# Optimization experiments

Measured on AMD Instinct MI355X. Metric: run time of the kernel, lower is better.

The kernel has to match this reference:

```python
import jax, jax.numpy as jnp
import numpy as np

TEMPERATURE_F = 0.5


def setup_inputs() -> dict:
    key = jax.random.key(0)
    k1, k2, k3, k4, k5 = jax.random.split(key, 5)
    B, D, K = 4096, 128, 8192
    return {
        "h_i": jax.random.normal(k1, (B, D), dtype=jnp.float32),
        "h_j": jax.random.normal(k2, (B, D), dtype=jnp.float32),
        "sub_graph": jax.random.uniform(k3, (B, K), dtype=jnp.float32),
        "sub_x": jax.random.normal(k4, (B, D), dtype=jnp.float32),
        "all_x": jax.random.normal(k5, (K, D), dtype=jnp.float32),
    }


def _forward_feature(h_i, h_j):
    # NT-Xent contrastive loss (CrossEntropyLoss with label 0, reduction='sum', /N).
    B = h_i.shape[0]
    N = 2 * B
    h = jnp.concatenate([h_i, h_j], axis=0)           # [N, D]
    sim = (h @ h.T) / TEMPERATURE_F                   # [N, N]
    idx = jnp.arange(N)
    pos = sim[idx, (idx + B) % N]                     # positives: diag(sim, +B) ++ diag(sim, -B)
    # logits row i = [pos_i] ++ {sim[i,j] : j != i, j != i±B}. Since pos_i == sim[i, i±B],
    # the logsumexp over that row equals logsumexp over sim[i,:] with only the diagonal removed.
    sim_nodiag = jnp.where(jnp.eye(N, dtype=bool), -jnp.inf, sim)
    lse = jax.nn.logsumexp(sim_nodiag, axis=1)        # [N]
    return jnp.sum(lse - pos) / N


def _graph_loss(sub_graph, sub_x, all_x):
    # trace(X^T diag(r) X) = sum_i r_i * ||X_i||^2 ; trace(A^T G B) = sum(G * (A B^T)) = sum((G B) * A)
    r = jnp.sum(sub_graph, axis=1)                    # [M]
    c = jnp.sum(sub_graph, axis=0)                    # [K]
    t1 = jnp.sum(r * jnp.sum(sub_x * sub_x, axis=1))
    t2 = jnp.sum(c * jnp.sum(all_x * all_x, axis=1))
    t3 = jnp.sum((sub_graph @ all_x) * sub_x)         # trace(sub_x^T G all_x)
    M, K = sub_graph.shape
    return (t1 + t2 - 2.0 * t3) / (M * K)


def reference(h_i, h_j, sub_graph, sub_x, all_x):
    contrastive = _forward_feature(h_i, h_j)
    graph = _graph_loss(sub_graph, sub_x, all_x)
    return contrastive + graph
```

## Files before the change

### kernel.cpp

```cpp
#include <hip/hip_runtime.h>
#include <hip/hip_bf16.h>

typedef __attribute__((ext_vector_type(4)))  float f32x4;
typedef __attribute__((ext_vector_type(16))) float f32x16;
typedef __attribute__((ext_vector_type(8)))  short s16x8;
typedef unsigned short u16;
typedef unsigned int u32;

#define ALPHA 1.6986436f
#define LN2F  0.69314718056f
#define COFF  128.0f

__device__ __forceinline__ u16 f2bf(float x) {
  union { float f; u32 u; } v; v.f = x;
  u32 r = v.u + 0x7fffu + ((v.u >> 16) & 1u);
  return (u16)(r >> 16);
}

#if __has_builtin(__builtin_amdgcn_exp2f)
__device__ __forceinline__ float fexp2(float x) { return __builtin_amdgcn_exp2f(x); }
#else
__device__ __forceinline__ float fexp2(float x) { return exp2f(x); }
#endif
#if __has_builtin(__builtin_amdgcn_logf)
__device__ __forceinline__ float flog2(float x) { return __builtin_amdgcn_logf(x); }
#else
__device__ __forceinline__ float flog2(float x) { return log2f(x); }
#endif

__device__ __forceinline__ s16x8 cvt8(float4 a, float4 b) {
  union { u32 w[4]; s16x8 v; } u;
  asm("v_cvt_pk_bf16_f32 %0, %1, %2" : "=v"(u.w[0]) : "v"(a.x), "v"(a.y));
  asm("v_cvt_pk_bf16_f32 %0, %1, %2" : "=v"(u.w[1]) : "v"(a.z), "v"(a.w));
  asm("v_cvt_pk_bf16_f32 %0, %1, %2" : "=v"(u.w[2]) : "v"(b.x), "v"(b.y));
  asm("v_cvt_pk_bf16_f32 %0, %1, %2" : "=v"(u.w[3]) : "v"(b.z), "v"(b.w));
  return u.v;
}

__device__ __forceinline__ f32x16 mfma32(s16x8 a, s16x8 b, f32x16 c) {
  return __builtin_amdgcn_mfma_f32_32x32x16_bf16(a, b, c, 0, 0, 0);
}
__device__ __forceinline__ f32x16 zero16() {
  f32x16 z;
#pragma unroll
  for (int i = 0; i < 16; ++i) z[i] = 0.f;
  return z;
}
__device__ __forceinline__ void gl16(const void* g, void* l) {
  __builtin_amdgcn_global_load_lds(
      (const __attribute__((address_space(1))) u32*)g,
      (__attribute__((address_space(3))) u32*)l, 16, 0, 0);
}

__global__ __launch_bounds__(256)
void prep_all(const float* __restrict__ h_i, const float* __restrict__ h_j,
              const float* __restrict__ all_x, const float* __restrict__ subx,
              u16* __restrict__ hbf, u16* __restrict__ axG,
              float* __restrict__ nall, float* __restrict__ nsub,
              float* __restrict__ pos4) {
  __shared__ float tile[64 * 132];
  int bid = blockIdx.x, tid = threadIdx.x;
  if (bid < 512) {
    int t = bid * 256 + tid;
    int row = t >> 4, kb = t & 15;
    const float* src = (row < 4096 ? h_i + (size_t)row * 128
                                   : h_j + (size_t)(row - 4096) * 128) + kb * 8;
    float4 f0 = *(const float4*)(src);
    float4 f1 = *(const float4*)(src + 4);
    float4 sa = {ALPHA * f0.x, ALPHA * f0.y, ALPHA * f0.z, ALPHA * f0.w};
    float4 sb = {ALPHA * f1.x, ALPHA * f1.y, ALPHA * f1.z, ALPHA * f1.w};
    s16x8 o = cvt8(sa, sb);
    char* dst = (char*)hbf + (size_t)row * 256 + ((kb * 16) ^ ((row & 7) << 4));
    *(s16x8*)dst = o;
    if (row < 4096) {
      const float* srcj = h_j + (size_t)row * 128 + kb * 8;
      float4 g0 = *(const float4*)(srcj);
      float4 g1 = *(const float4*)(srcj + 4);
      float dp = f0.x * g0.x + f0.y * g0.y + f0.z * g0.z + f0.w * g0.w
               + f1.x * g1.x + f1.y * g1.y + f1.z * g1.z + f1.w * g1.w;
      dp += __shfl_xor(dp, 1, 64);
      dp += __shfl_xor(dp, 2, 64);
      dp += __shfl_xor(dp, 4, 64);
      dp += __shfl_xor(dp, 8, 64);
      if ((tid & 15) == 0) pos4[row] = 2.0f * dp;
    }
  } else if (bid < 640) {
    int ab = bid - 512;
    int k0 = ab * 64;
#pragma unroll
    for (int j = 0; j < 8; ++j) {
      int idx = (j * 256 + tid) * 4;
      int kk = idx >> 7, d = idx & 127;
      *(float4*)&tile[kk * 132 + d] = *(const float4*)&all_x[(size_t)(k0 + kk) * 128 + d];
    }
    __syncthreads();
    {
      int kk = tid >> 2, q = tid & 3;
      float s = 0.f;
#pragma unroll
      for (int dd = 0; dd < 32; ++dd) { float v = tile[kk * 132 + q * 32 + dd]; s += v * v; }
      s += __shfl_xor(s, 1, 64);
      s += __shfl_xor(s, 2, 64);
      if (q == 0) nall[k0 + kk] = s;
    }
#pragma unroll
    for (int half = 0; half < 2; ++half) {
      int tgt = half * 256 + tid;
      int f = tgt >> 7, d = tgt & 127;
      int kc = ab * 4 + f;
      u16* dp = axG + (size_t)kc * 2048 + d * 16;
      s16x8 o0, o1;
#pragma unroll
      for (int kk = 0; kk < 8; ++kk) {
        o0[kk] = (short)f2bf(tile[(f * 16 + kk) * 132 + d]);
        o1[kk] = (short)f2bf(tile[(f * 16 + 8 + kk) * 132 + d]);
      }
      ((s16x8*)dp)[0] = o0; ((s16x8*)dp)[1] = o1;
    }
  } else {
    int i = (bid - 640) * 256 + tid;
    const float* p = subx + (size_t)i * 128;
    float s = 0.f;
#pragma unroll
    for (int c = 0; c < 32; ++c) {
      float4 v = ((const float4*)p)[c];
      s += v.x * v.x + v.y * v.y + v.z * v.z + v.w * v.w;
    }
    nsub[i] = s;
  }
}

__global__ __launch_bounds__(256, 3)
void contrast_k(const u16* __restrict__ hbf, float* __restrict__ spart) {
  __shared__ char clds[2][8192];
  int bid = blockIdx.x, tid = threadIdx.x;
  int lane = tid & 63, w = tid >> 6, il = lane & 31, hi = lane >> 5;
  int rt = bid >> 5, oct = bid & 31;
  int C0 = oct * 256;
  int rowbase = rt * 256 + w * 64;
  s16x8 bf0[8], bf1[8];
#pragma unroll
  for (int rs = 0; rs < 2; ++rs) {
    int r = rowbase + rs * 32 + il;
    const char* rp = (const char*)hbf + (size_t)r * 256;
    int sw = (r & 7) << 4;
#pragma unroll
    for (int ks = 0; ks < 8; ++ks) {
      s16x8 v = *(const s16x8*)(rp + ((ks * 32 + hi * 16) ^ sw));
      if (rs == 0) bf0[ks] = v; else bf1[ks] = v;
    }
  }
  float s0 = 0.f, s1 = 0.f;
  auto stage = [&](int buf, int t) {
    const char* src = (const char*)hbf + (size_t)(C0 + t * 32) * 256 + tid * 16;
    char* dst = &clds[buf][0] + tid * 16;
    gl16(src, dst);
    gl16(src + 4096, dst + 4096);
  };
  stage(0, 0);
  __syncthreads();
  int cur = 0;
  for (int t = 0; t < 8; ++t) {
    if (t < 7) stage(cur ^ 1, t + 1);
    const char* basep = &clds[cur][0];
    s16x8 af[8];
#pragma unroll
    for (int ks = 0; ks < 8; ++ks)
      af[ks] = *(const s16x8*)(basep + il * 256 + ((ks * 32 + hi * 16) ^ ((il & 7) << 4)));
    f32x16 A0 = zero16(), A1 = zero16();
#pragma unroll
    for (int ks = 0; ks < 8; ++ks) {
      A0 = mfma32(af[ks], bf0[ks], A0);
      A1 = mfma32(af[ks], bf1[ks], A1);
    }
    int cb = C0 + t * 32;
    bool d0 = (cb == rowbase), d1 = (cb == rowbase + 32);
#pragma unroll
    for (int r = 0; r < 16; ++r) {
      int jc = (r & 3) + 8 * (r >> 2) + 4 * hi;
      float t0 = fexp2(A0[r] - COFF);
      float t1 = fexp2(A1[r] - COFF);
      if (d0 && jc == il) t0 = 0.f;
      if (d1 && jc == il) t1 = 0.f;
      s0 += t0; s1 += t1;
    }
    __syncthreads();
    cur ^= 1;
  }
  s0 += __shfl_xor(s0, 32, 64);
  s1 += __shfl_xor(s1, 32, 64);
  if (hi == 0) {
    spart[oct * 8192 + rowbase + il]      = s0;
    spart[oct * 8192 + rowbase + 32 + il] = s1;
  }
}

__global__ __launch_bounds__(256, 4)
void graph_k(const float* __restrict__ G, const float* __restrict__ subx,
             const u16* __restrict__ axG, const float* __restrict__ nall,
             const float* __restrict__ nsub, float* __restrict__ gpart) {
  __shared__ u16 gtile[2][32][64];
  __shared__ float wsum[4];
  int bid = blockIdx.x, tid = threadIdx.x;
  int lane = tid & 63, w = tid >> 6, il = lane & 31, hi = lane >> 5;
  int mt = bid >> 3, kq = bid & 7;
  int i0 = mt * 32, i = i0 + il;
  int kbase = kq * 1024;
  int srow = tid >> 3, s8 = tid & 7;
  const float* gsrc = G + (size_t)(i0 + srow) * 8192 + kbase + s8 * 4;
  const float* nsrc = nall + kbase + s8 * 4;
  int sw_w = (srow & 7) << 4;
  int wo0 = ((s8 << 3))      ^ sw_w;
  int wo1 = (64 | (s8 << 3)) ^ sw_w;
  char* wb0 = (char*)&gtile[0][srow][0];
  char* wb1 = (char*)&gtile[1][srow][0];
  int swr = (il & 7) << 4;
  const char* aBase = (const char*)axG + (size_t)(kq * 64) * 4096
                    + (size_t)w * 1024 + il * 32 + hi * 16;

  f32x16 acc = zero16();
  float rsum = 0.f, nsum = 0.f;
  float4 gA0, gB0, nA0, nB0, gA1, gB1, nA1, nB1;

#define GISSUE(S, GA, GB, NA, NB)                                      \
  { const float* p_ = gsrc + (S) * 64;                                 \
    GA = *(const float4*)p_; GB = *(const float4*)(p_ + 32);           \
    const float* n_ = nsrc + (S) * 64;                                 \
    NA = *(const float4*)n_; NB = *(const float4*)(n_ + 32); }

#define GCOMMIT(GA, GB, NA, NB, DSTB)                                              \
  { u32 c0_, c1_, c2_, c3_;                                                        \
    asm("v_cvt_pk_bf16_f32 %0, %1, %2" : "=v"(c0_) : "v"(GA.x), "v"(GA.y));        \
    asm("v_cvt_pk_bf16_f32 %0, %1, %2" : "=v"(c1_) : "v"(GA.z), "v"(GA.w));        \
    asm("v_cvt_pk_bf16_f32 %0, %1, %2" : "=v"(c2_) : "v"(GB.x), "v"(GB.y));        \
    asm("v_cvt_pk_bf16_f32 %0, %1, %2" : "=v"(c3_) : "v"(GB.z), "v"(GB.w));        \
    *(uint2*)((DSTB) + wo0) = make_uint2(c0_, c1_);                                \
    *(uint2*)((DSTB) + wo1) = make_uint2(c2_, c3_);                                \
    rsum += GA.x + GA.y + GA.z + GA.w + GB.x + GB.y + GB.z + GB.w;                 \
    nsum += GA.x * NA.x + GA.y * NA.y + GA.z * NA.z + GA.w * NA.w                  \
          + GB.x * NB.x + GB.y * NB.y + GB.z * NB.z + GB.w * NB.w; }

#define GBAR()                                                \
  asm volatile("s_waitcnt lgkmcnt(0)" ::: "memory");          \
  __builtin_amdgcn_sched_barrier(0);                          \
  __builtin_amdgcn_s_barrier();                               \
  __builtin_amdgcn_sched_barrier(0);

#define GSTEP(S, GA_I, GB_I, NA_I, NB_I, GA_O, GB_O, NA_O, NB_O, CURB, OTHB)       \
  { const char* aB_ = aBase + (size_t)((S) * 4) * 4096;                            \
    s16x8 aF0 = *(const s16x8*)(aB_);                                              \
    s16x8 aF1 = *(const s16x8*)(aB_ + 4096);                                       \
    s16x8 aF2 = *(const s16x8*)(aB_ + 8192);                                       \
    s16x8 aF3 = *(const s16x8*)(aB_ + 12288);                                      \
    if ((S) < 14) GISSUE((S) + 2, GA_I, GB_I, NA_I, NB_I);                         \
    const char* rb_ = (const char*)&gtile[CURB][il][0];                            \
    s16x8 B0 = *(const s16x8*)(rb_ + ((0 * 32 + hi * 16) ^ swr));                  \
    s16x8 B1 = *(const s16x8*)(rb_ + ((1 * 32 + hi * 16) ^ swr));                  \
    s16x8 B2 = *(const s16x8*)(rb_ + ((2 * 32 + hi * 16) ^ swr));                  \
    s16x8 B3 = *(const s16x8*)(rb_ + ((3 * 32 + hi * 16) ^ swr));                  \
    acc = mfma32(aF0, B0, acc);                                                    \
    acc = mfma32(aF1, B1, acc);                                                    \
    acc = mfma32(aF2, B2, acc);                                                    \
    acc = mfma32(aF3, B3, acc);                                                    \
    if ((S) < 15) GCOMMIT(GA_O, GB_O, NA_O, NB_O, (OTHB));                         \
    GBAR(); }

  GISSUE(0, gA0, gB0, nA0, nB0);
  GISSUE(1, gA1, gB1, nA1, nB1);
  GCOMMIT(gA0, gB0, nA0, nB0, wb0);
  GBAR();

  for (int sp = 0; sp < 8; ++sp) {
    int s = sp * 2;
    GSTEP(s,     gA0, gB0, nA0, nB0, gA1, gB1, nA1, nB1, 0, wb1);
    GSTEP(s + 1, gA1, gB1, nA1, nB1, gA0, gB0, nA0, nB0, 1, wb0);
  }
#undef GSTEP
#undef GBAR
#undef GCOMMIT
#undef GISSUE

  float p = rsum * nsub[i0 + srow] + nsum;
  const float* sxr = subx + (size_t)i * 128 + w * 32 + hi * 4;
#pragma unroll
  for (int rq = 0; rq < 4; ++rq) {
    float4 sx = *(const float4*)(sxr + rq * 8);
    p -= 2.0f * (acc[rq * 4 + 0] * sx.x + acc[rq * 4 + 1] * sx.y +
                 acc[rq * 4 + 2] * sx.z + acc[rq * 4 + 3] * sx.w);
  }
#pragma unroll
  for (int d = 1; d < 64; d <<= 1) p += __shfl_xor(p, d, 64);
  if (lane == 0) wsum[w] = p;
  __syncthreads();
  if (tid == 0) gpart[bid] = wsum[0] + wsum[1] + wsum[2] + wsum[3];
}

__global__ __launch_bounds__(256)
void epilogue1(const float* __restrict__ spart, const float* __restrict__ pos4,
               float* __restrict__ cpart) {
  int tid = threadIdx.x;
  int row = blockIdx.x * 256 + tid;
  float S = 0.f;
#pragma unroll
  for (int o = 0; o < 32; ++o) S += spart[o * 8192 + row];
  float c = LN2F * (COFF + flog2(S)) - pos4[row & 4095];
#pragma unroll
  for (int d = 1; d < 64; d <<= 1) c += __shfl_xor(c, d, 64);
  __shared__ float ws4[4];
  int l = tid & 63, w = tid >> 6;
  if (l == 0) ws4[w] = c;
  __syncthreads();
  if (tid == 0) cpart[blockIdx.x] = ws4[0] + ws4[1] + ws4[2] + ws4[3];
}

__global__ __launch_bounds__(256)
void final_sum(const float* __restrict__ cpart, const float* __restrict__ gpart,
               float* __restrict__ out) {
  int tid = threadIdx.x;
  double gd = 0.0;
  for (int idx = tid; idx < 1024; idx += 256) gd += (double)gpart[idx];
  double cd = (tid < 32) ? (double)cpart[tid] : 0.0;
#pragma unroll
  for (int d = 1; d < 64; d <<= 1) {
    cd += __shfl_xor(cd, d, 64);
    gd += __shfl_xor(gd, d, 64);
  }
  __shared__ double wc[4], wg[4];
  int l = tid & 63, w = tid >> 6;
  if (l == 0) { wc[w] = cd; wg[w] = gd; }
  __syncthreads();
  if (tid == 0) {
    double C = wc[0] + wc[1] + wc[2] + wc[3];
    double Gs = wg[0] + wg[1] + wg[2] + wg[3];
    out[0] = (float)(C / 8192.0 + Gs / (4096.0 * 8192.0));
  }
}

extern "C" void kernel_launch(void* const* d_in, const int* in_sizes, int n_in,
                              void* d_out, int out_size, void* d_ws, size_t ws_size,
                              hipStream_t stream) {
  const float* h_i = (const float*)d_in[0];
  const float* h_j = (const float*)d_in[1];
  const float* G   = (const float*)d_in[2];
  const float* sx  = (const float*)d_in[3];
  const float* ax  = (const float*)d_in[4];
  char* ws = (char*)d_ws;
  u16*   hbf   = (u16*)(ws);
  u16*   axG   = (u16*)(ws + 2097152);
  float* nall  = (float*)(ws + 4194304);
  float* nsub  = (float*)(ws + 4227072);
  float* pos4  = (float*)(ws + 4243456);
  float* spart = (float*)(ws + 4259840);
  float* gpart = (float*)(ws + 5308416);
  float* cpart = (float*)(ws + 5312512);
  float* out = (float*)d_out;

  prep_all<<<dim3(656), dim3(256), 0, stream>>>(h_i, h_j, ax, sx, hbf, axG, nall, nsub, pos4);
  contrast_k<<<dim3(1024), dim3(256), 0, stream>>>(hbf, spart);
  graph_k<<<dim3(1024), dim3(256), 0, stream>>>(G, sx, axG, nall, nsub, gpart);
  epilogue1<<<dim3(32), dim3(256), 0, stream>>>(spart, pos4, cpart);
  final_sum<<<dim3(1), dim3(256), 0, stream>>>(cpart, gpart, out);
}
```

Baseline: 65.94 us.

## Fuse contrastive and graph kernels into one interleaved launch

Merges the compute-bound contrastive similarity kernel and the memory-bound graph kernel into a single launch, alternating blocks between the two roles so the MFMA/exp work overlaps with streaming the large graph matrix. The node-norm slice is staged once into LDS instead of being reloaded from global memory on every step. The per-element diagonal masking is skipped on tiles that do not contain the diagonal. The fused kernel uses a shared LDS pool and the stricter launch bound of three blocks per SM, which may reduce occupancy for the graph half.

Measured after the change: 61.89 us. 6.1% less time.

```diff
diff --git a/kernel.cpp b/kernel.cpp
--- a/kernel.cpp
+++ b/kernel.cpp
@@ -131,168 +131,180 @@
 }
 
 __global__ __launch_bounds__(256, 3)
-void contrast_k(const u16* __restrict__ hbf, float* __restrict__ spart) {
-  __shared__ char clds[2][8192];
+void main_fused(const float* __restrict__ G, const float* __restrict__ subx,
+                const u16* __restrict__ axG, const float* __restrict__ nall,
+                const float* __restrict__ nsub, const u16* __restrict__ hbf,
+                float* __restrict__ spart, float* __restrict__ gpart) {
+  __shared__ char pool[16640];
   int bid = blockIdx.x, tid = threadIdx.x;
   int lane = tid & 63, w = tid >> 6, il = lane & 31, hi = lane >> 5;
-  int rt = bid >> 5, oct = bid & 31;
-  int C0 = oct * 256;
-  int rowbase = rt * 256 + w * 64;
-  s16x8 bf0[8], bf1[8];
-#pragma unroll
-  for (int rs = 0; rs < 2; ++rs) {
-    int r = rowbase + rs * 32 + il;
-    const char* rp = (const char*)hbf + (size_t)r * 256;
-    int sw = (r & 7) << 4;
-#pragma unroll
-    for (int ks = 0; ks < 8; ++ks) {
-      s16x8 v = *(const s16x8*)(rp + ((ks * 32 + hi * 16) ^ sw));
-      if (rs == 0) bf0[ks] = v; else bf1[ks] = v;
-    }
-  }
-  float s0 = 0.f, s1 = 0.f;
-  auto stage = [&](int buf, int t) {
-    const char* src = (const char*)hbf + (size_t)(C0 + t * 32) * 256 + tid * 16;
-    char* dst = &clds[buf][0] + tid * 16;
-    gl16(src, dst);
-    gl16(src + 4096, dst + 4096);
-  };
-  stage(0, 0);
-  __syncthreads();
-  int cur = 0;
-  for (int t = 0; t < 8; ++t) {
-    if (t < 7) stage(cur ^ 1, t + 1);
-    const char* basep = &clds[cur][0];
-    s16x8 af[8];
-#pragma unroll
-    for (int ks = 0; ks < 8; ++ks)
-      af[ks] = *(const s16x8*)(basep + il * 256 + ((ks * 32 + hi * 16) ^ ((il & 7) << 4)));
-    f32x16 A0 = zero16(), A1 = zero16();
-#pragma unroll
-    for (int ks = 0; ks < 8; ++ks) {
-      A0 = mfma32(af[ks], bf0[ks], A0);
-      A1 = mfma32(af[ks], bf1[ks], A1);
-    }
-    int cb = C0 + t * 32;
-    bool d0 = (cb == rowbase), d1 = (cb == rowbase + 32);
-#pragma unroll
-    for (int r = 0; r < 16; ++r) {
-      int jc = (r & 3) + 8 * (r >> 2) + 4 * hi;
-      float t0 = fexp2(A0[r] - COFF);
-      float t1 = fexp2(A1[r] - COFF);
-      if (d0 && jc == il) t0 = 0.f;
-      if (d1 && jc == il) t1 = 0.f;
-      s0 += t0; s1 += t1;
-    }
+
+  if ((bid & 1) == 0) {
+    int gid = bid >> 1;
+    int mt = gid >> 3, kq = gid & 7;
+    int i0 = mt * 32;
+    int kbase = kq * 1024;
+    int srow = tid >> 3, s8 = tid & 7;
+    u16 (*gtile)[32][64] = (u16(*)[32][64])pool;
+    float* nll  = (float*)(pool + 8192);
+    float* wsum = (float*)(pool + 12288);
+    const float* gsrc = G + (size_t)(i0 + srow) * 8192 + kbase + s8 * 4;
+    int sw_w = (srow & 7) << 4;
+    int wo0 = ((s8 << 3))      ^ sw_w;
+    int wo1 = (64 | (s8 << 3)) ^ sw_w;
+    char* wb0 = (char*)&gtile[0][srow][0];
+    char* wb1 = (char*)&gtile[1][srow][0];
+    int swr = (il & 7) << 4;
+    const char* aBase = (const char*)axG + (size_t)(kq * 64) * 4096
+                      + (size_t)w * 1024 + il * 32 + hi * 16;
+
+    *(float4*)&nll[tid * 4] = *(const float4*)&nall[kbase + tid * 4];
     __syncthreads();
-    cur ^= 1;
-  }
-  s0 += __shfl_xor(s0, 32, 64);
-  s1 += __shfl_xor(s1, 32, 64);
-  if (hi == 0) {
-    spart[oct * 8192 + rowbase + il]      = s0;
-    spart[oct * 8192 + rowbase + 32 + il] = s1;
-  }
-}
-
-__global__ __launch_bounds__(256, 4)
-void graph_k(const float* __restrict__ G, const float* __restrict__ subx,
-             const u16* __restrict__ axG, const float* __restrict__ nall,
-             const float* __restrict__ nsub, float* __restrict__ gpart) {
-  __shared__ u16 gtile[2][32][64];
-  __shared__ float wsum[4];
-  int bid = blockIdx.x, tid = threadIdx.x;
-  int lane = tid & 63, w = tid >> 6, il = lane & 31, hi = lane >> 5;
-  int mt = bid >> 3, kq = bid & 7;
-  int i0 = mt * 32, i = i0 + il;
-  int kbase = kq * 1024;
-  int srow = tid >> 3, s8 = tid & 7;
-  const float* gsrc = G + (size_t)(i0 + srow) * 8192 + kbase + s8 * 4;
-  const float* nsrc = nall + kbase + s8 * 4;
-  int sw_w = (srow & 7) << 4;
-  int wo0 = ((s8 << 3))      ^ sw_w;
-  int wo1 = (64 | (s8 << 3)) ^ sw_w;
-  char* wb0 = (char*)&gtile[0][srow][0];
-  char* wb1 = (char*)&gtile[1][srow][0];
-  int swr = (il & 7) << 4;
-  const char* aBase = (const char*)axG + (size_t)(kq * 64) * 4096
-                    + (size_t)w * 1024 + il * 32 + hi * 16;
-
-  f32x16 acc = zero16();
-  float rsum = 0.f, nsum = 0.f;
-  float4 gA0, gB0, nA0, nB0, gA1, gB1, nA1, nB1;
-
-#define GISSUE(S, GA, GB, NA, NB)                                      \
-  { const float* p_ = gsrc + (S) * 64;                                 \
-    GA = *(const float4*)p_; GB = *(const float4*)(p_ + 32);           \
-    const float* n_ = nsrc + (S) * 64;                                 \
-    NA = *(const float4*)n_; NB = *(const float4*)(n_ + 32); }
-
-#define GCOMMIT(GA, GB, NA, NB, DSTB)                                              \
-  { u32 c0_, c1_, c2_, c3_;                                                        \
-    asm("v_cvt_pk_bf16_f32 %0, %1, %2" : "=v"(c0_) : "v"(GA.x), "v"(GA.y));        \
-    asm("v_cvt_pk_bf16_f32 %0, %1, %2" : "=v"(c1_) : "v"(GA.z), "v"(GA.w));        \
-    asm("v_cvt_pk_bf16_f32 %0, %1, %2" : "=v"(c2_) : "v"(GB.x), "v"(GB.y));        \
-    asm("v_cvt_pk_bf16_f32 %0, %1, %2" : "=v"(c3_) : "v"(GB.z), "v"(GB.w));        \
-    *(uint2*)((DSTB) + wo0) = make_uint2(c0_, c1_);                                \
-    *(uint2*)((DSTB) + wo1) = make_uint2(c2_, c3_);                                \
-    rsum += GA.x + GA.y + GA.z + GA.w + GB.x + GB.y + GB.z + GB.w;                 \
-    nsum += GA.x * NA.x + GA.y * NA.y + GA.z * NA.z + GA.w * NA.w                  \
-          + GB.x * NB.x + GB.y * NB.y + GB.z * NB.z + GB.w * NB.w; }
+
+    f32x16 acc = zero16();
+    float rsum = 0.f, nsum = 0.f;
+    float4 gA0, gB0, gA1, gB1;
+
+#define GISSUE(S, GA, GB)                                              \
+    { const float* p_ = gsrc + (S) * 64;                               \
+      GA = *(const float4*)p_; GB = *(const float4*)(p_ + 32); }
+
+#define GCOMMIT(GA, GB, DSTB, SC)                                                  \
+    { u32 c0_, c1_, c2_, c3_;                                                      \
+      asm("v_cvt_pk_bf16_f32 %0, %1, %2" : "=v"(c0_) : "v"(GA.x), "v"(GA.y));      \
+      asm("v_cvt_pk_bf16_f32 %0, %1, %2" : "=v"(c1_) : "v"(GA.z), "v"(GA.w));      \
+      asm("v_cvt_pk_bf16_f32 %0, %1, %2" : "=v"(c2_) : "v"(GB.x), "v"(GB.y));      \
+      asm("v_cvt_pk_bf16_f32 %0, %1, %2" : "=v"(c3_) : "v"(GB.z), "v"(GB.w));      \
+      *(uint2*)((DSTB) + wo0) = make_uint2(c0_, c1_);                              \
+      *(uint2*)((DSTB) + wo1) = make_uint2(c2_, c3_);                              \
+      float4 NA = *(const float4*)&nll[(SC) * 64 + s8 * 4];                        \
+      float4 NB = *(const float4*)&nll[(SC) * 64 + s8 * 4 + 32];                   \
+      rsum += GA.x + GA.y + GA.z + GA.w + GB.x + GB.y + GB.z + GB.w;               \
+      nsum += GA.x * NA.x + GA.y * NA.y + GA.z * NA.z + GA.w * NA.w                \
+            + GB.x * NB.x + GB.y * NB.y + GB.z * NB.z + GB.w * NB.w; }
 
 #define GBAR()                                                \
-  asm volatile("s_waitcnt lgkmcnt(0)" ::: "memory");          \
-  __builtin_amdgcn_sched_barrier(0);                          \
-  __builtin_amdgcn_s_barrier();                               \
-  __builtin_amdgcn_sched_barrier(0);
-
-#define GSTEP(S, GA_I, GB_I, NA_I, NB_I, GA_O, GB_O, NA_O, NB_O, CURB, OTHB)       \
-  { const char* aB_ = aBase + (size_t)((S) * 4) * 4096;                            \
-    s16x8 aF0 = *(const s16x8*)(aB_);                                              \
-    s16x8 aF1 = *(const s16x8*)(aB_ + 4096);                                       \
-    s16x8 aF2 = *(const s16x8*)(aB_ + 8192);                                       \
-    s16x8 aF3 = *(const s16x8*)(aB_ + 12288);                                      \
-    if ((S) < 14) GISSUE((S) + 2, GA_I, GB_I, NA_I, NB_I);                         \
-    const char* rb_ = (const char*)&gtile[CURB][il][0];                            \
-    s16x8 B0 = *(const s16x8*)(rb_ + ((0 * 32 + hi * 16) ^ swr));                  \
-    s16x8 B1 = *(const s16x8*)(rb_ + ((1 * 32 + hi * 16) ^ swr));                  \
-    s16x8 B2 = *(const s16x8*)(rb_ + ((2 * 32 + hi * 16) ^ swr));                  \
-    s16x8 B3 = *(const s16x8*)(rb_ + ((3 * 32 + hi * 16) ^ swr));                  \
-    acc = mfma32(aF0, B0, acc);                                                    \
-    acc = mfma32(aF1, B1, acc);                                                    \
-    acc = mfma32(aF2, B2, acc);                                                    \
-    acc = mfma32(aF3, B3, acc);                                                    \
-    if ((S) < 15) GCOMMIT(GA_O, GB_O, NA_O, NB_O, (OTHB));                         \
-    GBAR(); }
-
-  GISSUE(0, gA0, gB0, nA0, nB0);
-  GISSUE(1, gA1, gB1, nA1, nB1);
-  GCOMMIT(gA0, gB0, nA0, nB0, wb0);
-  GBAR();
-
-  for (int sp = 0; sp < 8; ++sp) {
-    int s = sp * 2;
-    GSTEP(s,     gA0, gB0, nA0, nB0, gA1, gB1, nA1, nB1, 0, wb1);
-    GSTEP(s + 1, gA1, gB1, nA1, nB1, gA0, gB0, nA0, nB0, 1, wb0);
-  }
+    asm volatile("s_waitcnt lgkmcnt(0)" ::: "memory");        \
+    __builtin_amdgcn_sched_barrier(0);                        \
+    __builtin_amdgcn_s_barrier();                             \
+    __builtin_amdgcn_sched_barrier(0);
+
+#define GSTEP(S, GA_I, GB_I, GA_O, GB_O, CURB, OTHB)                               \
+    { const char* aB_ = aBase + (size_t)((S) * 4) * 4096;                          \
+      s16x8 aF0 = *(const s16x8*)(aB_);                                            \
+      s16x8 aF1 = *(const s16x8*)(aB_ + 4096);                                     \
+      s16x8 aF2 = *(const s16x8*)(aB_ + 8192);                                     \
+      s16x8 aF3 = *(const s16x8*)(aB_ + 12288);                                    \
+      if ((S) < 14) GISSUE((S) + 2, GA_I, GB_I);                                   \
+      const char* rb_ = (const char*)&gtile[CURB][il][0];                          \
+      s16x8 B0 = *(const s16x8*)(rb_ + ((0 * 32 + hi * 16) ^ swr));                \
+      s16x8 B1 = *(const s16x8*)(rb_ + ((1 * 32 + hi * 16) ^ swr));                \
+      s16x8 B2 = *(const s16x8*)(rb_ + ((2 * 32 + hi * 16) ^ swr));                \
+      s16x8 B3 = *(const s16x8*)(rb_ + ((3 * 32 + hi * 16) ^ swr));                \
+      acc = mfma32(aF0, B0, acc);                                                  \
+      acc = mfma32(aF1, B1, acc);                                                  \
+      acc = mfma32(aF2, B2, acc);                                                  \
+      acc = mfma32(aF3, B3, acc);                                                  \
+      if ((S) < 15) GCOMMIT(GA_O, GB_O, (OTHB), (S) + 1);                          \
+      GBAR(); }
+
+    GISSUE(0, gA0, gB0);
+    GISSUE(1, gA1, gB1);
+    GCOMMIT(gA0, gB0, wb0, 0);
+    GBAR();
+    for (int sp = 0; sp < 8; ++sp) {
+      int s = sp * 2;
+      GSTEP(s,     gA0, gB0, gA1, gB1, 0, wb1);
+      GSTEP(s + 1, gA1, gB1, gA0, gB0, 1, wb0);
+    }
 #undef GSTEP
 #undef GBAR
 #undef GCOMMIT
 #undef GISSUE
 
-  float p = rsum * nsub[i0 + srow] + nsum;
-  const float* sxr = subx + (size_t)i * 128 + w * 32 + hi * 4;
-#pragma unroll
-  for (int rq = 0; rq < 4; ++rq) {
-    float4 sx = *(const float4*)(sxr + rq * 8);
-    p -= 2.0f * (acc[rq * 4 + 0] * sx.x + acc[rq * 4 + 1] * sx.y +
-                 acc[rq * 4 + 2] * sx.z + acc[rq * 4 + 3] * sx.w);
+    float p = rsum * nsub[i0 + srow] + nsum;
+    const float* sxr = subx + (size_t)(i0 + il) * 128 + w * 32 + hi * 4;
+#pragma unroll
+    for (int rq = 0; rq < 4; ++rq) {
+      float4 sx = *(const float4*)(sxr + rq * 8);
+      p -= 2.0f * (acc[rq * 4 + 0] * sx.x + acc[rq * 4 + 1] * sx.y +
+                   acc[rq * 4 + 2] * sx.z + acc[rq * 4 + 3] * sx.w);
+    }
+#pragma unroll
+    for (int d = 1; d < 64; d <<= 1) p += __shfl_xor(p, d, 64);
+    if (lane == 0) wsum[w] = p;
+    __syncthreads();
+    if (tid == 0) gpart[gid] = wsum[0] + wsum[1] + wsum[2] + wsum[3];
+  } else {
+    int cid = bid >> 1;
+    int rt = cid >> 5, oct = cid & 31;
+    int C0 = oct * 256;
+    int rowbase = rt * 256 + w * 64;
+    char (*clds)[8192] = (char(*)[8192])pool;
+    s16x8 bf0[8], bf1[8];
+#pragma unroll
+    for (int rs = 0; rs < 2; ++rs) {
+      int r = rowbase + rs * 32 + il;
+      const char* rp = (const char*)hbf + (size_t)r * 256;
+      int sw = (r & 7) << 4;
+#pragma unroll
+      for (int ks = 0; ks < 8; ++ks) {
+        s16x8 v = *(const s16x8*)(rp + ((ks * 32 + hi * 16) ^ sw));
+        if (rs == 0) bf0[ks] = v; else bf1[ks] = v;
+      }
+    }
+    float s0 = 0.f, s1 = 0.f;
+    auto stage = [&](int buf, int t) {
+      const char* src = (const char*)hbf + (size_t)(C0 + t * 32) * 256 + tid * 16;
+      char* dst = &clds[buf][0] + tid * 16;
+      gl16(src, dst);
+      gl16(src + 4096, dst + 4096);
+    };
+    stage(0, 0);
+    __syncthreads();
+    int cur = 0;
+    for (int t = 0; t < 8; ++t) {
+      if (t < 7) stage(cur ^ 1, t + 1);
+      const char* basep = &clds[cur][0];
+      s16x8 af[8];
+#pragma unroll
+      for (int ks = 0; ks < 8; ++ks)
+        af[ks] = *(const s16x8*)(basep + il * 256 + ((ks * 32 + hi * 16) ^ ((il & 7) << 4)));
+      f32x16 A0 = zero16(), A1 = zero16();
+#pragma unroll
+      for (int ks = 0; ks < 8; ++ks) {
+        A0 = mfma32(af[ks], bf0[ks], A0);
+        A1 = mfma32(af[ks], bf1[ks], A1);
+      }
+      int cb = C0 + t * 32;
+      bool d0 = (cb == rowbase), d1 = (cb == rowbase + 32);
+      if (!(d0 | d1)) {
+#pragma unroll
+        for (int r = 0; r < 16; ++r) {
+          s0 += fexp2(A0[r] - COFF);
+          s1 += fexp2(A1[r] - COFF);
+        }
+      } else {
+#pragma unroll
+        for (int r = 0; r < 16; ++r) {
+          int jc = (r & 3) + 8 * (r >> 2) + 4 * hi;
+          float t0 = fexp2(A0[r] - COFF);
+          float t1 = fexp2(A1[r] - COFF);
+          if (d0 && jc == il) t0 = 0.f;
+          if (d1 && jc == il) t1 = 0.f;
+          s0 += t0; s1 += t1;
+        }
+      }
+      __syncthreads();
+      cur ^= 1;
+    }
+    s0 += __shfl_xor(s0, 32, 64);
+    s1 += __shfl_xor(s1, 32, 64);
+    if (hi == 0) {
+      spart[oct * 8192 + rowbase + il]      = s0;
+      spart[oct * 8192 + rowbase + 32 + il] = s1;
+    }
   }
-#pragma unroll
-  for (int d = 1; d < 64; d <<= 1) p += __shfl_xor(p, d, 64);
-  if (lane == 0) wsum[w] = p;
-  __syncthreads();
-  if (tid == 0) gpart[bid] = wsum[0] + wsum[1] + wsum[2] + wsum[3];
 }
 
 __global__ __launch_bounds__(256)
@@ -356,8 +368,7 @@
   float* out = (float*)d_out;
 
   prep_all<<<dim3(656), dim3(256), 0, stream>>>(h_i, h_j, ax, sx, hbf, axG, nall, nsub, pos4);
-  contrast_k<<<dim3(1024), dim3(256), 0, stream>>>(hbf, spart);
-  graph_k<<<dim3(1024), dim3(256), 0, stream>>>(G, sx, axG, nall, nsub, gpart);
+  main_fused<<<dim3(2048), dim3(256), 0, stream>>>(G, sx, axG, nall, nsub, hbf, spart, gpart);
   epilogue1<<<dim3(32), dim3(256), 0, stream>>>(spart, pos4, cpart);
   final_sum<<<dim3(1), dim3(256), 0, stream>>>(cpart, gpart, out);
 }
```

## Restructure graph loss as per-tile sub_x·all_x^T MFMA weighted by G

Applied to the files above, without the earlier changes.

The graph kernel no longer computes G@all_x with G staged in LDS. It instead computes E = sub_x·all_x^T tiles with bf16 MFMA and accumulates sum G*(||x_i||^2 + ||a_k||^2 - 2E) directly from fp32 G loaded in registers, removing the LDS G tile and its barriers. Prep now writes bf16 sub_x and a k-major bf16 all_x layout. The contrastive kernel also skips the diagonal-mask branch for non-diagonal tiles and drops its occupancy hint. The exchange is more MFMA work (inner dimension D instead of K) and strided per-lane G loads.

Result: faster. 60.13 us (-8.8%).

```diff
diff --git a/kernel.cpp b/kernel.cpp
--- a/kernel.cpp
+++ b/kernel.cpp
@@ -55,10 +55,9 @@
 __global__ __launch_bounds__(256)
 void prep_all(const float* __restrict__ h_i, const float* __restrict__ h_j,
               const float* __restrict__ all_x, const float* __restrict__ subx,
-              u16* __restrict__ hbf, u16* __restrict__ axG,
+              u16* __restrict__ hbf, u16* __restrict__ axKT, u16* __restrict__ sxb,
               float* __restrict__ nall, float* __restrict__ nsub,
               float* __restrict__ pos4) {
-  __shared__ float tile[64 * 132];
   int bid = blockIdx.x, tid = threadIdx.x;
   if (bid < 512) {
     int t = bid * 256 + tid;
@@ -86,51 +85,49 @@
     }
   } else if (bid < 640) {
     int ab = bid - 512;
-    int k0 = ab * 64;
-#pragma unroll
-    for (int j = 0; j < 8; ++j) {
-      int idx = (j * 256 + tid) * 4;
-      int kk = idx >> 7, d = idx & 127;
-      *(float4*)&tile[kk * 132 + d] = *(const float4*)&all_x[(size_t)(k0 + kk) * 128 + d];
-    }
-    __syncthreads();
     {
-      int kk = tid >> 2, q = tid & 3;
+      int kk = ab * 64 + (tid >> 2), q = tid & 3;
+      const float* p = all_x + (size_t)kk * 128 + q * 32;
       float s = 0.f;
 #pragma unroll
-      for (int dd = 0; dd < 32; ++dd) { float v = tile[kk * 132 + q * 32 + dd]; s += v * v; }
+      for (int c = 0; c < 8; ++c) {
+        float4 v = ((const float4*)p)[c];
+        s += v.x * v.x + v.y * v.y + v.z * v.z + v.w * v.w;
+      }
       s += __shfl_xor(s, 1, 64);
       s += __shfl_xor(s, 2, 64);
-      if (q == 0) nall[k0 + kk] = s;
-    }
-#pragma unroll
-    for (int half = 0; half < 2; ++half) {
-      int tgt = half * 256 + tid;
-      int f = tgt >> 7, d = tgt & 127;
-      int kc = ab * 4 + f;
-      u16* dp = axG + (size_t)kc * 2048 + d * 16;
-      s16x8 o0, o1;
-#pragma unroll
-      for (int kk = 0; kk < 8; ++kk) {
-        o0[kk] = (short)f2bf(tile[(f * 16 + kk) * 132 + d]);
-        o1[kk] = (short)f2bf(tile[(f * 16 + 8 + kk) * 132 + d]);
-      }
-      ((s16x8*)dp)[0] = o0; ((s16x8*)dp)[1] = o1;
+      if (q == 0) nall[kk] = s;
+    }
+#pragma unroll
+    for (int j = 0; j < 2; ++j) {
+      int c = ab * 512 + tid * 2 + j;
+      int k = c >> 3, dc = c & 7;
+      const float* p = all_x + (size_t)k * 128 + dc * 16;
+      float4 a0 = ((const float4*)p)[0];
+      float4 a1 = ((const float4*)p)[1];
+      float4 a2 = ((const float4*)p)[2];
+      float4 a3 = ((const float4*)p)[3];
+      *(s16x8*)((char*)axKT + (size_t)dc * 262144 + (size_t)k * 32)      = cvt8(a0, a1);
+      *(s16x8*)((char*)axKT + (size_t)dc * 262144 + (size_t)k * 32 + 16) = cvt8(a2, a3);
     }
   } else {
-    int i = (bid - 640) * 256 + tid;
-    const float* p = subx + (size_t)i * 128;
-    float s = 0.f;
-#pragma unroll
-    for (int c = 0; c < 32; ++c) {
-      float4 v = ((const float4*)p)[c];
-      s += v.x * v.x + v.y * v.y + v.z * v.z + v.w * v.w;
-    }
-    nsub[i] = s;
-  }
-}
-
-__global__ __launch_bounds__(256, 3)
+    int t = (bid - 640) * 256 + tid;
+    int row = t >> 4, kb = t & 15;
+    const float* src = subx + (size_t)row * 128 + kb * 8;
+    float4 f0 = *(const float4*)(src);
+    float4 f1 = *(const float4*)(src + 4);
+    *(s16x8*)((char*)sxb + (size_t)row * 256 + kb * 16) = cvt8(f0, f1);
+    float dp = f0.x * f0.x + f0.y * f0.y + f0.z * f0.z + f0.w * f0.w
+             + f1.x * f1.x + f1.y * f1.y + f1.z * f1.z + f1.w * f1.w;
+    dp += __shfl_xor(dp, 1, 64);
+    dp += __shfl_xor(dp, 2, 64);
+    dp += __shfl_xor(dp, 4, 64);
+    dp += __shfl_xor(dp, 8, 64);
+    if ((tid & 15) == 0) nsub[row] = dp;
+  }
+}
+
+__global__ __launch_bounds__(256)
 void contrast_k(const u16* __restrict__ hbf, float* __restrict__ spart) {
   __shared__ char clds[2][8192];
   int bid = blockIdx.x, tid = threadIdx.x;
@@ -175,14 +172,22 @@
     }
     int cb = C0 + t * 32;
     bool d0 = (cb == rowbase), d1 = (cb == rowbase + 32);
-#pragma unroll
-    for (int r = 0; r < 16; ++r) {
-      int jc = (r & 3) + 8 * (r >> 2) + 4 * hi;
-      float t0 = fexp2(A0[r] - COFF);
-      float t1 = fexp2(A1[r] - COFF);
-      if (d0 && jc == il) t0 = 0.f;
-      if (d1 && jc == il) t1 = 0.f;
-      s0 += t0; s1 += t1;
+    if (!(d0 | d1)) {
+#pragma unroll
+      for (int r = 0; r < 16; ++r) {
+        s0 += fexp2(A0[r] - COFF);
+        s1 += fexp2(A1[r] - COFF);
+      }
+    } else {
+#pragma unroll
+      for (int r = 0; r < 16; ++r) {
+        int jc = (r & 3) + 8 * (r >> 2) + 4 * hi;
+        float t0 = fexp2(A0[r] - COFF);
+        float t1 = fexp2(A1[r] - COFF);
+        if (d0 && jc == il) t0 = 0.f;
+        if (d1 && jc == il) t1 = 0.f;
+        s0 += t0; s1 += t1;
+      }
     }
     __syncthreads();
     cur ^= 1;
@@ -195,102 +200,88 @@
   }
 }
 
-__global__ __launch_bounds__(256, 4)
-void graph_k(const float* __restrict__ G, const float* __restrict__ subx,
-             const u16* __restrict__ axG, const float* __restrict__ nall,
+__global__ __launch_bounds__(256)
+void graph_k(const float* __restrict__ G, const u16* __restrict__ sxb,
+             const u16* __restrict__ axKT, const float* __restrict__ nall,
              const float* __restrict__ nsub, float* __restrict__ gpart) {
-  __shared__ u16 gtile[2][32][64];
   __shared__ float wsum[4];
   int bid = blockIdx.x, tid = threadIdx.x;
   int lane = tid & 63, w = tid >> 6, il = lane & 31, hi = lane >> 5;
-  int mt = bid >> 3, kq = bid & 7;
-  int i0 = mt * 32, i = i0 + il;
-  int kbase = kq * 1024;
-  int srow = tid >> 3, s8 = tid & 7;
-  const float* gsrc = G + (size_t)(i0 + srow) * 8192 + kbase + s8 * 4;
-  const float* nsrc = nall + kbase + s8 * 4;
-  int sw_w = (srow & 7) << 4;
-  int wo0 = ((s8 << 3))      ^ sw_w;
-  int wo1 = (64 | (s8 << 3)) ^ sw_w;
-  char* wb0 = (char*)&gtile[0][srow][0];
-  char* wb1 = (char*)&gtile[1][srow][0];
-  int swr = (il & 7) << 4;
-  const char* aBase = (const char*)axG + (size_t)(kq * 64) * 4096
-                    + (size_t)w * 1024 + il * 32 + hi * 16;
-
-  f32x16 acc = zero16();
-  float rsum = 0.f, nsum = 0.f;
-  float4 gA0, gB0, nA0, nB0, gA1, gB1, nA1, nB1;
-
-#define GISSUE(S, GA, GB, NA, NB)                                      \
-  { const float* p_ = gsrc + (S) * 64;                                 \
-    GA = *(const float4*)p_; GB = *(const float4*)(p_ + 32);           \
-    const float* n_ = nsrc + (S) * 64;                                 \
-    NA = *(const float4*)n_; NB = *(const float4*)(n_ + 32); }
-
-#define GCOMMIT(GA, GB, NA, NB, DSTB)                                              \
-  { u32 c0_, c1_, c2_, c3_;                                                        \
-    asm("v_cvt_pk_bf16_f32 %0, %1, %2" : "=v"(c0_) : "v"(GA.x), "v"(GA.y));        \
-    asm("v_cvt_pk_bf16_f32 %0, %1, %2" : "=v"(c1_) : "v"(GA.z), "v"(GA.w));        \
-    asm("v_cvt_pk_bf16_f32 %0, %1, %2" : "=v"(c2_) : "v"(GB.x), "v"(GB.y));        \
-    asm("v_cvt_pk_bf16_f32 %0, %1, %2" : "=v"(c3_) : "v"(GB.z), "v"(GB.w));        \
-    *(uint2*)((DSTB) + wo0) = make_uint2(c0_, c1_);                                \
-    *(uint2*)((DSTB) + wo1) = make_uint2(c2_, c3_);                                \
-    rsum += GA.x + GA.y + GA.z + GA.w + GB.x + GB.y + GB.z + GB.w;                 \
-    nsum += GA.x * NA.x + GA.y * NA.y + GA.z * NA.z + GA.w * NA.w                  \
-          + GB.x * NB.x + GB.y * NB.y + GB.z * NB.z + GB.w * NB.w; }
-
-#define GBAR()                                                \
-  asm volatile("s_waitcnt lgkmcnt(0)" ::: "memory");          \
-  __builtin_amdgcn_sched_barrier(0);                          \
-  __builtin_amdgcn_s_barrier();                               \
-  __builtin_amdgcn_sched_barrier(0);
-
-#define GSTEP(S, GA_I, GB_I, NA_I, NB_I, GA_O, GB_O, NA_O, NB_O, CURB, OTHB)       \
-  { const char* aB_ = aBase + (size_t)((S) * 4) * 4096;                            \
-    s16x8 aF0 = *(const s16x8*)(aB_);                                              \
-    s16x8 aF1 = *(const s16x8*)(aB_ + 4096);                                       \
-    s16x8 aF2 = *(const s16x8*)(aB_ + 8192);                                       \
-    s16x8 aF3 = *(const s16x8*)(aB_ + 12288);                                      \
-    if ((S) < 14) GISSUE((S) + 2, GA_I, GB_I, NA_I, NB_I);                         \
-    const char* rb_ = (const char*)&gtile[CURB][il][0];                            \
-    s16x8 B0 = *(const s16x8*)(rb_ + ((0 * 32 + hi * 16) ^ swr));                  \
-    s16x8 B1 = *(const s16x8*)(rb_ + ((1 * 32 + hi * 16) ^ swr));                  \
-    s16x8 B2 = *(const s16x8*)(rb_ + ((2 * 32 + hi * 16) ^ swr));                  \
-    s16x8 B3 = *(const s16x8*)(rb_ + ((3 * 32 + hi * 16) ^ swr));                  \
-    acc = mfma32(aF0, B0, acc);                                                    \
-    acc = mfma32(aF1, B1, acc);                                                    \
-    acc = mfma32(aF2, B2, acc);                                                    \
-    acc = mfma32(aF3, B3, acc);                                                    \
-    if ((S) < 15) GCOMMIT(GA_O, GB_O, NA_O, NB_O, (OTHB));                         \
-    GBAR(); }
-
-  GISSUE(0, gA0, gB0, nA0, nB0);
-  GISSUE(1, gA1, gB1, nA1, nB1);
-  GCOMMIT(gA0, gB0, nA0, nB0, wb0);
-  GBAR();
-
-  for (int sp = 0; sp < 8; ++sp) {
-    int s = sp * 2;
-    GSTEP(s,     gA0, gB0, nA0, nB0, gA1, gB1, nA1, nB1, 0, wb1);
-    GSTEP(s + 1, gA1, gB1, nA1, nB1, gA0, gB0, nA0, nB0, 1, wb0);
-  }
+  int rb = bid >> 2, kq = bid & 3;
+  int i0 = rb * 32;
+  int k0w = kq * 2048 + w * 512;
+
+  s16x8 A[8];
+#pragma unroll
+  for (int dc = 0; dc < 8; ++dc)
+    A[dc] = *(const s16x8*)((const char*)sxb + (size_t)(i0 + il) * 256 + dc * 32 + hi * 16);
+
+  float ns[16];
+#pragma unroll
+  for (int r = 0; r < 16; ++r)
+    ns[r] = nsub[i0 + (r & 3) + 8 * (r >> 2) + 4 * hi];
+
+  const char* aktB = (const char*)axKT + il * 32 + hi * 16;
+  const float* gB = G + (size_t)i0 * 8192 + il;
+  const float* nlB = nall + il;
+
+  float s = 0.f;
+  float g0[16], g1[16], g2[16];
+  float nk0, nk1, nk2;
+  s16x8 B0[8], B1[8];
+
+#define GLOAD(T, GR, NK)                                                     \
+  { int k_ = k0w + (T) * 32;                                                 \
+    _Pragma("unroll")                                                        \
+    for (int r = 0; r < 16; ++r)                                             \
+      GR[r] = gB[(size_t)(((r & 3) + 8 * (r >> 2) + 4 * hi) * 8192 + k_)];   \
+    NK = nlB[k_]; }
+
+#define BLOAD(T, BR)                                                         \
+  { int k_ = k0w + (T) * 32;                                                 \
+    _Pragma("unroll")                                                        \
+    for (int dc = 0; dc < 8; ++dc)                                           \
+      BR[dc] = *(const s16x8*)(aktB + (size_t)dc * 262144 + (size_t)k_ * 32); }
+
+#define GSTEP(T, GR, NK, BR)                                                 \
+  { f32x16 E = zero16();                                                     \
+    _Pragma("unroll")                                                        \
+    for (int dc = 0; dc < 8; ++dc) E = mfma32(A[dc], BR[dc], E);             \
+    _Pragma("unroll")                                                        \
+    for (int r = 0; r < 16; ++r)                                             \
+      s = fmaf(GR[r], fmaf(-2.f, E[r], ns[r] + NK), s);                      \
+    if ((T) + 2 <= 15) BLOAD((T) + 2, BR);                                   \
+    if ((T) + 3 <= 15) GLOAD((T) + 3, GR, NK); }
+
+  GLOAD(0, g0, nk0);
+  BLOAD(0, B0);
+  GLOAD(1, g1, nk1);
+  BLOAD(1, B1);
+  GLOAD(2, g2, nk2);
+
+  GSTEP(0,  g0, nk0, B0)
+  GSTEP(1,  g1, nk1, B1)
+  GSTEP(2,  g2, nk2, B0)
+  GSTEP(3,  g0, nk0, B1)
+  GSTEP(4,  g1, nk1, B0)
+  GSTEP(5,  g2, nk2, B1)
+  GSTEP(6,  g0, nk0, B0)
+  GSTEP(7,  g1, nk1, B1)
+  GSTEP(8,  g2, nk2, B0)
+  GSTEP(9,  g0, nk0, B1)
+  GSTEP(10, g1, nk1, B0)
+  GSTEP(11, g2, nk2, B1)
+  GSTEP(12, g0, nk0, B0)
+  GSTEP(13, g1, nk1, B1)
+  GSTEP(14, g2, nk2, B0)
+  GSTEP(15, g0, nk0, B1)
 #undef GSTEP
-#undef GBAR
-#undef GCOMMIT
-#undef GISSUE
-
-  float p = rsum * nsub[i0 + srow] + nsum;
-  const float* sxr = subx + (size_t)i * 128 + w * 32 + hi * 4;
-#pragma unroll
-  for (int rq = 0; rq < 4; ++rq) {
-    float4 sx = *(const float4*)(sxr + rq * 8);
-    p -= 2.0f * (acc[rq * 4 + 0] * sx.x + acc[rq * 4 + 1] * sx.y +
-                 acc[rq * 4 + 2] * sx.z + acc[rq * 4 + 3] * sx.w);
-  }
-#pragma unroll
-  for (int d = 1; d < 64; d <<= 1) p += __shfl_xor(p, d, 64);
-  if (lane == 0) wsum[w] = p;
+#undef BLOAD
+#undef GLOAD
+
+#pragma unroll
+  for (int d = 1; d < 64; d <<= 1) s += __shfl_xor(s, d, 64);
+  if (lane == 0) wsum[w] = s;
   __syncthreads();
   if (tid == 0) gpart[bid] = wsum[0] + wsum[1] + wsum[2] + wsum[3];
 }
@@ -318,7 +309,7 @@
                float* __restrict__ out) {
   int tid = threadIdx.x;
   double gd = 0.0;
-  for (int idx = tid; idx < 1024; idx += 256) gd += (double)gpart[idx];
+  for (int idx = tid; idx < 512; idx += 256) gd += (double)gpart[idx];
   double cd = (tid < 32) ? (double)cpart[tid] : 0.0;
 #pragma unroll
   for (int d = 1; d < 64; d <<= 1) {
@@ -346,18 +337,20 @@
   const float* ax  = (const float*)d_in[4];
   char* ws = (char*)d_ws;
   u16*   hbf   = (u16*)(ws);
-  u16*   axG   = (u16*)(ws + 2097152);
-  float* nall  = (float*)(ws + 4194304);
-  float* nsub  = (float*)(ws + 4227072);
-  float* pos4  = (float*)(ws + 4243456);
-  float* spart = (float*)(ws + 4259840);
-  float* gpart = (float*)(ws + 5308416);
-  float* cpart = (float*)(ws + 5312512);
+  u16*   axKT  = (u16*)(ws + 2097152);
+  u16*   sxb   = (u16*)(ws + 4194304);
+  float* nall  = (float*)(ws + 5242880);
+  float* nsub  = (float*)(ws + 5275648);
+  float* pos4  = (float*)(ws + 5292032);
+  float* spart = (float*)(ws + 5308416);
+  float* gpart = (float*)(ws + 6356992);
+  float* cpart = (float*)(ws + 6359040);
   float* out = (float*)d_out;
 
-  prep_all<<<dim3(656), dim3(256), 0, stream>>>(h_i, h_j, ax, sx, hbf, axG, nall, nsub, pos4);
+  prep_all<<<dim3(896), dim3(256), 0, stream>>>(h_i, h_j, ax, sx, hbf, axKT, sxb,
+                                                nall, nsub, pos4);
   contrast_k<<<dim3(1024), dim3(256), 0, stream>>>(hbf, spart);
-  graph_k<<<dim3(1024), dim3(256), 0, stream>>>(G, sx, axG, nall, nsub, gpart);
+  graph_k<<<dim3(512), dim3(256), 0, stream>>>(G, sxb, axKT, nall, nsub, gpart);
   epilogue1<<<dim3(32), dim3(256), 0, stream>>>(spart, pos4, cpart);
   final_sum<<<dim3(1), dim3(256), 0, stream>>>(cpart, gpart, out);
 }
```
